# Performance work log

Hardware: AMD Instinct MI355X
Metric: run time of the kernel (lower is better)

The kernel has to match this reference:

```python
import jax, jax.numpy as jnp
import numpy as np

D_MODEL = 1024
N_HEADS = 16
HEAD_DIM = D_MODEL // N_HEADS
BATCH = 4
SEQ = 2048


def setup_inputs() -> dict:
    key = jax.random.key(0)
    k_x, k_wqkv, k_bqkv, k_wo, k_bo = jax.random.split(key, 5)
    x = jax.random.normal(k_x, (BATCH, SEQ, D_MODEL), dtype=jnp.float32)
    # causal mask: True = masked (upper triangle, excluding diagonal)
    mask = jnp.triu(jnp.ones((SEQ, SEQ), dtype=bool), k=1)
    lim = 1.0 / np.sqrt(D_MODEL)
    w_qkv = jax.random.uniform(k_wqkv, (D_MODEL, 3 * D_MODEL), jnp.float32, -lim, lim)
    b_qkv = jax.random.uniform(k_bqkv, (3 * D_MODEL,), jnp.float32, -lim, lim)
    w_out = jax.random.uniform(k_wo, (D_MODEL, D_MODEL), jnp.float32, -lim, lim)
    b_out = jax.random.uniform(k_bo, (D_MODEL,), jnp.float32, -lim, lim)
    return {"x": x, "mask": mask, "w_qkv": w_qkv, "b_qkv": b_qkv,
            "w_out": w_out, "b_out": b_out}


def reference(x, mask, w_qkv, b_qkv, w_out, b_out):
    b, s, _ = x.shape
    scale = HEAD_DIM ** -0.5
    qkv = x @ w_qkv + b_qkv                          # [b, s, 3*d]
    qkv = qkv.reshape(b, s, 3, N_HEADS, HEAD_DIM)
    qkv = jnp.transpose(qkv, (2, 0, 3, 1, 4))        # [3, b, h, s, hd]
    q, k, v = qkv[0], qkv[1], qkv[2]
    attn = jnp.einsum('bhqd,bhkd->bhqk', q, k) * scale
    attn = jnp.where(mask, -jnp.inf, attn)
    attn = jax.nn.softmax(attn, axis=-1)
    out = jnp.einsum('bhqk,bhkd->bhqd', attn, v)     # [b, h, s, hd]
    out = jnp.transpose(out, (0, 2, 1, 3)).reshape(b, s, D_MODEL)
    return out @ w_out + b_out
```

## Files before the change

kernel.cpp:

```cpp
#include <hip/hip_runtime.h>
#include <stdint.h>

typedef unsigned short u16;
typedef __attribute__((ext_vector_type(8))) short short8;
typedef __attribute__((ext_vector_type(4))) float f32x4;
typedef __attribute__((ext_vector_type(16))) float f32x16;

#define DEV static __device__ __forceinline__

#define QSCALE 0.18033688011112042f

DEV float fast_exp2(float x) { return __builtin_amdgcn_exp2f(x); }

DEV float bf2f(u16 u) { union { uint32_t i; float f; } x; x.i = ((uint32_t)u) << 16; return x.f; }
DEV u16 f2bf(float f) {
  union { float f; uint32_t i; } x; x.f = f;
  uint32_t r = x.i + 0x7FFFu + ((x.i >> 16) & 1u);
  return (u16)(r >> 16);
}
DEV uint32_t pk_bf16(float lo, float hi) {
  uint32_t r;
  asm("v_cvt_pk_bf16_f32 %0, %1, %2" : "=v"(r) : "v"(lo), "v"(hi));
  return r;
}

DEV void async_copy16(void* lds_dst, const void* gsrc) {
  typedef __attribute__((address_space(1))) void* gp_t;
  typedef __attribute__((address_space(3))) void* lp_t;
  __builtin_amdgcn_global_load_lds((gp_t)(uintptr_t)gsrc,
                                   (lp_t)(uint32_t)(uintptr_t)lds_dst, 16, 0, 0);
}

#define BUF_BYTES 49152

DEV void stage_slot(const u16* __restrict__ A, const u16* __restrict__ Bt,
                    int m0, int n0, int k0, uint8_t* buf, int tid) {
  uint8_t* As = buf;
  uint8_t* Bs = buf + 32768;
#pragma unroll
  for (int i = 0; i < 4; ++i) {
    int c = i * 512 + tid;
    int r = c >> 3;
    int ks = (c & 7) ^ (r & 7);
    async_copy16(As + c * 16, A + (size_t)(m0 + r) * 1024 + k0 + ks * 8);
  }
#pragma unroll
  for (int i = 0; i < 2; ++i) {
    int c = i * 512 + tid;
    int r = c >> 3;
    int ks = (c & 7) ^ (r & 7);
    async_copy16(Bs + c * 16, Bt + (size_t)(n0 + r) * 1024 + k0 + ks * 8);
  }
}

DEV void gemm256_core(const u16* __restrict__ A, const u16* __restrict__ Bt,
                      int m0, int n0, uint8_t* lds,
                      f32x4 (&acc)[4][4], int wave, int lane, int tid) {
  const int wm = (wave >> 1) * 64, wn = (wave & 1) * 64;
#pragma unroll
  for (int mf = 0; mf < 4; ++mf)
#pragma unroll
    for (int nf = 0; nf < 4; ++nf)
      acc[mf][nf] = (f32x4){0.f, 0.f, 0.f, 0.f};

  stage_slot(A, Bt, m0, n0, 0,  lds,             tid);
  stage_slot(A, Bt, m0, n0, 64, lds + BUF_BYTES, tid);
  asm volatile("s_waitcnt vmcnt(6)" ::: "memory");
  __builtin_amdgcn_s_barrier();

#pragma unroll 1
  for (int kt = 0; kt < 16; ++kt) {
    const uint8_t* Ab = lds + (kt & 1) * BUF_BYTES;
    const uint8_t* Bb = Ab + 32768;

    short8 a0[4], b0[4], a1[4], b1[4];
#pragma unroll
    for (int f = 0; f < 4; ++f) {
      int ra = wm + f * 16 + (lane & 15);
      int rb = wn + f * 16 + (lane & 15);
      a0[f] = *(const short8*)(Ab + ra * 128 + (((lane >> 4) ^ (ra & 7)) << 4));
      b0[f] = *(const short8*)(Bb + rb * 128 + (((lane >> 4) ^ (rb & 7)) << 4));
    }
#pragma unroll
    for (int f = 0; f < 4; ++f) {
      int ra = wm + f * 16 + (lane & 15);
      int rb = wn + f * 16 + (lane & 15);
      a1[f] = *(const short8*)(Ab + ra * 128 + (((4 + (lane >> 4)) ^ (ra & 7)) << 4));
      b1[f] = *(const short8*)(Bb + rb * 128 + (((4 + (lane >> 4)) ^ (rb & 7)) << 4));
    }

    asm volatile("s_waitcnt lgkmcnt(8)" ::: "memory");
    __builtin_amdgcn_sched_barrier(0);
    __builtin_amdgcn_s_setprio(1);
#pragma unroll
    for (int mf = 0; mf < 4; ++mf)
#pragma unroll
      for (int nf = 0; nf < 4; ++nf)
        acc[mf][nf] = __builtin_amdgcn_mfma_f32_16x16x32_bf16(a0[mf], b0[nf],
                                                              acc[mf][nf], 0, 0, 0);
    __builtin_amdgcn_s_setprio(0);

    asm volatile("s_waitcnt lgkmcnt(0)" ::: "memory");
    __builtin_amdgcn_sched_barrier(0);
    __builtin_amdgcn_s_barrier();

    if (kt + 2 < 16)
      stage_slot(A, Bt, m0, n0, (kt + 2) * 64, lds + (kt & 1) * BUF_BYTES, tid);

    __builtin_amdgcn_s_setprio(1);
#pragma unroll
    for (int mf = 0; mf < 4; ++mf)
#pragma unroll
      for (int nf = 0; nf < 4; ++nf)
        acc[mf][nf] = __builtin_amdgcn_mfma_f32_16x16x32_bf16(a1[mf], b1[nf],
                                                              acc[mf][nf], 0, 0, 0);
    __builtin_amdgcn_s_setprio(0);

    if (kt + 2 < 16) asm volatile("s_waitcnt vmcnt(6)" ::: "memory");
    else             asm volatile("s_waitcnt vmcnt(0)" ::: "memory");
    __builtin_amdgcn_s_barrier();
  }
}

__global__ __launch_bounds__(512, 2) void k_gemm_qkv(
    const u16* __restrict__ X, const u16* __restrict__ WT, const float* __restrict__ bias,
    u16* __restrict__ Q, u16* __restrict__ Kv, u16* __restrict__ Vt) {
  __shared__ __attribute__((aligned(16))) uint8_t lds[2 * BUF_BYTES];
  const int tid = threadIdx.x, lane = tid & 63, wave = tid >> 6;
  const int wm = (wave >> 1) * 64, wn = (wave & 1) * 64;
  const int m0 = blockIdx.x * 256, n0 = blockIdx.y * 128;
  f32x4 acc[4][4];
  gemm256_core(X, WT, m0, n0, lds, acc, wave, lane, tid);
#pragma unroll
  for (int nf = 0; nf < 4; ++nf) {
    int n = n0 + wn + nf * 16 + (lane & 15);
    float bv = bias[n];
    int which = n >> 10, h = (n >> 6) & 15, hd = n & 63;
    if (which == 2) {
#pragma unroll
      for (int mf = 0; mf < 4; ++mf) {
        int m = m0 + wm + mf * 16 + (lane >> 4) * 4;
        int b = m >> 11, s = m & 2047;
        u16 tmp[4];
#pragma unroll
        for (int rg = 0; rg < 4; ++rg) tmp[rg] = f2bf(acc[mf][nf][rg] + bv);
        *(uint64_t*)(Vt + ((size_t)(b * 16 + h) * 64 + hd) * 2048 + s) = *(const uint64_t*)tmp;
      }
    } else {
      u16* base = (which == 0) ? Q : Kv;
      const float mul = (which == 0) ? QSCALE : 1.0f;
#pragma unroll
      for (int mf = 0; mf < 4; ++mf)
#pragma unroll
        for (int rg = 0; rg < 4; ++rg) {
          int m = m0 + wm + mf * 16 + (lane >> 4) * 4 + rg;
          int b = m >> 11, s = m & 2047;
          base[((size_t)(b * 16 + h) * 2048 + s) * 64 + hd] = f2bf((acc[mf][nf][rg] + bv) * mul);
        }
    }
  }
}

__global__ __launch_bounds__(512, 2) void k_gemm_out(
    const u16* __restrict__ A, const u16* __restrict__ WT, const float* __restrict__ bias,
    float* __restrict__ Out) {
  __shared__ __attribute__((aligned(16))) uint8_t lds[2 * BUF_BYTES];
  const int tid = threadIdx.x, lane = tid & 63, wave = tid >> 6;
  const int wm = (wave >> 1) * 64, wn = (wave & 1) * 64;
  const int m0 = blockIdx.x * 256, n0 = blockIdx.y * 128;
  f32x4 acc[4][4];
  gemm256_core(A, WT, m0, n0, lds, acc, wave, lane, tid);
#pragma unroll
  for (int nf = 0; nf < 4; ++nf) {
    int n = n0 + wn + nf * 16 + (lane & 15);
    float bv = bias[n];
#pragma unroll
    for (int mf = 0; mf < 4; ++mf)
#pragma unroll
      for (int rg = 0; rg < 4; ++rg) {
        int m = m0 + wm + mf * 16 + (lane >> 4) * 4 + rg;
        Out[(size_t)m * 1024 + n] = acc[mf][nf][rg] + bv;
      }
  }
}

__global__ __launch_bounds__(256) void k_cvt_x(const float* __restrict__ src,
                                               u16* __restrict__ dst, int n8) {
  int i = blockIdx.x * 256 + threadIdx.x;
  if (i >= n8) return;
  float4 a = *(const float4*)(src + (size_t)i * 8);
  float4 b = *(const float4*)(src + (size_t)i * 8 + 4);
  u16 tmp[8] = {f2bf(a.x), f2bf(a.y), f2bf(a.z), f2bf(a.w),
                f2bf(b.x), f2bf(b.y), f2bf(b.z), f2bf(b.w)};
  *(short8*)(dst + (size_t)i * 8) = *(const short8*)tmp;
}

__global__ __launch_bounds__(256) void k_transpose_f32(
    const float* __restrict__ src, u16* __restrict__ dst, int R, int C) {
  __shared__ u16 tile[64][72];
  const int tr = blockIdx.x * 64, tc = blockIdx.y * 64;
  for (int c = threadIdx.x; c < 1024; c += 256) {
    int r = c >> 4, c4 = (c & 15) * 4;
    float4 v = *(const float4*)(src + (size_t)(tr + r) * C + tc + c4);
    tile[r][c4 + 0] = f2bf(v.x); tile[r][c4 + 1] = f2bf(v.y);
    tile[r][c4 + 2] = f2bf(v.z); tile[r][c4 + 3] = f2bf(v.w);
  }
  __syncthreads();
  for (int c = threadIdx.x; c < 512; c += 256) {
    int oc = c >> 3, r8 = (c & 7) * 8;
    u16 tmp[8];
#pragma unroll
    for (int i = 0; i < 8; ++i) tmp[i] = tile[r8 + i][oc];
    *(short8*)(dst + (size_t)(tc + oc) * R + tr + r8) = *(const short8*)tmp;
  }
}

DEV void stage_tile(const u16* __restrict__ Kg, const u16* __restrict__ Vg,
                    uint8_t* kb, uint8_t* vb, int t, int tid) {
#pragma unroll
  for (int i = 0; i < 2; ++i) {
    int c = i * 256 + tid;
    int r = c >> 3;
    int ks = (c & 7) ^ (r & 7);
    async_copy16(kb + c * 16, Kg + (size_t)(t * 64 + r) * 64 + ks * 8);
    async_copy16(vb + c * 16, Vg + (size_t)r * 2048 + t * 64 + ks * 8);
  }
}

__global__ __launch_bounds__(256, 2) void k_attn(
    const u16* __restrict__ Q, const u16* __restrict__ K,
    const u16* __restrict__ Vt, u16* __restrict__ O) {
  __shared__ __attribute__((aligned(16))) uint8_t kbuf[2][8192];
  __shared__ __attribute__((aligned(16))) uint8_t vbuf[2][8192];
  const int tid = threadIdx.x;
  const int lane = tid & 63;
  const int wave = tid >> 6;
  const int q32 = lane & 31, hv = lane >> 5;
  const float NEG_INF = -__builtin_inff();

  int L = blockIdx.x;
  int bh = (L & 7) * 8 + ((L >> 3) >> 3);
  int pair = (L >> 3) & 7;
  const int b = bh >> 4, h = bh & 15;
  const size_t hb = (size_t)bh * (2048 * 64);
  const u16* Qg = Q + hb;
  const u16* Kg = K + hb;
  const u16* Vg = Vt + hb;

#pragma unroll 1
  for (int which = 0; which < 2; ++which) {
    const int s = which ? (15 - pair) : pair;
    const int nt = 2 * (s + 1);
    const int qbase = s * 128 + wave * 32;
    const int qg = qbase + q32;
    const int my_nt = ((qbase + 31) >> 6) + 1;

    short8 qf[4];
#pragma unroll
    for (int dblk = 0; dblk < 4; ++dblk)
      qf[dblk] = *(const short8*)(Qg + (size_t)qg * 64 + dblk * 16 + hv * 8);

    f32x16 oacc[2] = {};
    float mrun = NEG_INF, lrun = 0.f;

    stage_tile(Kg, Vg, kbuf[0], vbuf[0], 0, tid);
    __syncthreads();

#pragma unroll 1
    for (int t = 0; t < nt; ++t) {
      const int cur = t & 1;
      if (t + 1 < nt) stage_tile(Kg, Vg, kbuf[cur ^ 1], vbuf[cur ^ 1], t + 1, tid);

      if (t < my_nt) {
        const uint8_t* kb = kbuf[cur];
        const uint8_t* vb = vbuf[cur];

        f32x16 sa0 = {}, sa1 = {};
        __builtin_amdgcn_s_setprio(1);
#pragma unroll
        for (int dblk = 0; dblk < 4; ++dblk) {
          short8 kf0 = *(const short8*)(kb + q32 * 128 + (((dblk * 2 + hv) ^ (q32 & 7)) << 4));
          short8 kf1 = *(const short8*)(kb + (32 + q32) * 128 + (((dblk * 2 + hv) ^ (q32 & 7)) << 4));
          sa0 = __builtin_amdgcn_mfma_f32_32x32x16_bf16(kf0, qf[dblk], sa0, 0, 0, 0);
          sa1 = __builtin_amdgcn_mfma_f32_32x32x16_bf16(kf1, qf[dblk], sa1, 0, 0, 0);
        }
        __builtin_amdgcn_s_setprio(0);

        float sv[32];
#pragma unroll
        for (int r = 0; r < 16; ++r) { sv[r] = sa0[r]; sv[16 + r] = sa1[r]; }
        if (t * 64 + 63 > qbase) {
#pragma unroll
          for (int r = 0; r < 16; ++r) {
            int kl = (r & 3) + 8 * (r >> 2) + 4 * hv;
            if (t * 64 + kl > qg)      sv[r]      = NEG_INF;
            if (t * 64 + 32 + kl > qg) sv[16 + r] = NEG_INF;
          }
        }

        float mloc = fmaxf(sv[0], sv[1]);
#pragma unroll
        for (int r = 2; r < 32; ++r) mloc = fmaxf(mloc, sv[r]);
        float mtile = fmaxf(mloc, __shfl_xor(mloc, 32, 64));
        if (!__all(mtile <= mrun + 8.f)) {
          float mnew = fmaxf(mrun, mtile);
          float corr = fast_exp2(mrun - mnew);
          mrun = mnew;
          lrun *= corr;
#pragma unroll
          for (int r = 0; r < 16; ++r) { oacc[0][r] *= corr; oacc[1][r] *= corr; }
        }
        float ls = 0.f;
#pragma unroll
        for (int r = 0; r < 32; ++r) { sv[r] = fast_exp2(sv[r] - mrun); ls += sv[r]; }
        ls += __shfl_xor(ls, 32, 64);
        lrun += ls;

        __builtin_amdgcn_s_setprio(1);
#pragma unroll
        for (int ksub = 0; ksub < 2; ++ksub) {
#pragma unroll
          for (int kb2 = 0; kb2 < 2; ++kb2) {
            const int rb = ksub * 16 + kb2 * 8;
            uint32_t pA = pk_bf16(sv[rb + 0], sv[rb + 1]);
            uint32_t pB = pk_bf16(sv[rb + 2], sv[rb + 3]);
            uint32_t pC = pk_bf16(sv[rb + 4], sv[rb + 5]);
            uint32_t pD = pk_bf16(sv[rb + 6], sv[rb + 7]);
            uint32_t X = hv ? pA : pC;
            uint32_t Y = hv ? pB : pD;
            uint32_t sX = (uint32_t)__shfl_xor((int)X, 32, 64);
            uint32_t sY = (uint32_t)__shfl_xor((int)Y, 32, 64);
            union { uint32_t u[4]; short8 s8; } pu;
            pu.u[0] = hv ? sX : pA;
            pu.u[1] = hv ? sY : pB;
            pu.u[2] = hv ? pC : sX;
            pu.u[3] = hv ? pD : sY;
            const int kblk = ksub * 2 + kb2;
            short8 vf0 = *(const short8*)(vb + q32 * 128 + (((kblk * 2 + hv) ^ (q32 & 7)) << 4));
            short8 vf1 = *(const short8*)(vb + (32 + q32) * 128 + (((kblk * 2 + hv) ^ (q32 & 7)) << 4));
            oacc[0] = __builtin_amdgcn_mfma_f32_32x32x16_bf16(vf0, pu.s8, oacc[0], 0, 0, 0);
            oacc[1] = __builtin_amdgcn_mfma_f32_32x32x16_bf16(vf1, pu.s8, oacc[1], 0, 0, 0);
          }
        }
        __builtin_amdgcn_s_setprio(0);
      }

      __syncthreads();
    }

    float rl = 1.0f / lrun;
    u16* orow = O + ((size_t)(b * 2048 + qg)) * 1024 + h * 64;
#pragma unroll
    for (int dt = 0; dt < 2; ++dt)
#pragma unroll
      for (int g = 0; g < 4; ++g) {
        int dbase = dt * 32 + 8 * g + 4 * hv;
        u16 tmp[4];
#pragma unroll
        for (int j2 = 0; j2 < 4; ++j2) tmp[j2] = f2bf(oacc[dt][4 * g + j2] * rl);
        *(uint64_t*)(orow + dbase) = *(const uint64_t*)tmp;
      }
  }
}

extern "C" void kernel_launch(void* const* d_in, const int* in_sizes, int n_in,
                              void* d_out, int out_size, void* d_ws, size_t ws_size,
                              hipStream_t stream) {
  const float* x     = (const float*)d_in[0];
  const float* w_qkv = (const float*)d_in[2];
  const float* b_qkv = (const float*)d_in[3];
  const float* w_out = (const float*)d_in[4];
  const float* b_out = (const float*)d_in[5];
  float* out = (float*)d_out;
  uint8_t* ws = (uint8_t*)d_ws;

  u16* wqkvT = (u16*)(ws);
  u16* woutT = (u16*)(ws +  6291456);
  u16* Xb    = (u16*)(ws +  8388608);
  u16* Qb    = (u16*)(ws + 25165824);
  u16* Kb    = (u16*)(ws + 41943040);
  u16* Vtb   = (u16*)(ws + 58720256);
  u16* AO    = Xb;

  k_cvt_x<<<dim3(4096), 256, 0, stream>>>(x, Xb, 1048576);
  k_transpose_f32<<<dim3(16, 48), 256, 0, stream>>>(w_qkv, wqkvT, 1024, 3072);
  k_transpose_f32<<<dim3(16, 16), 256, 0, stream>>>(w_out, woutT, 1024, 1024);
  k_gemm_qkv<<<dim3(32, 24), 512, 0, stream>>>(Xb, wqkvT, b_qkv, Qb, Kb, Vtb);
  k_attn<<<dim3(512), 256, 0, stream>>>(Qb, Kb, Vtb, AO);
  k_gemm_out<<<dim3(32, 8), 512, 0, stream>>>(AO, woutT, b_out, out);
}
```

Before: 160.6 us.

## Use simpler 128x128 single-buffered GEMM core for QKV projection

Replaces the QKV projection's 256x128 double-buffered, prefetching GEMM core with a new 128x128-tile core. The new core uses 256 threads and a single LDS buffer with a barrier on each side of every K-step, and the grid doubles along M. It drops the software pipelining and the wave priority hints, so global loads no longer overlap MFMA work, in exchange for more blocks and less LDS per block.

```diff
diff --git a/kernel.cpp b/kernel.cpp
--- a/kernel.cpp
+++ b/kernel.cpp
@@ -29,6 +29,49 @@
   typedef __attribute__((address_space(3))) void* lp_t;
   __builtin_amdgcn_global_load_lds((gp_t)(uintptr_t)gsrc,
                                    (lp_t)(uint32_t)(uintptr_t)lds_dst, 16, 0, 0);
+}
+
+DEV void gemm_bt_core(const u16* __restrict__ A, const u16* __restrict__ Bt, int K,
+                      int m0, int n0, uint8_t* As, uint8_t* Bs,
+                      f32x4 (&acc)[4][4], int wave, int lane, int wm, int wn) {
+#pragma unroll
+  for (int mt = 0; mt < 4; ++mt)
+#pragma unroll
+    for (int nt = 0; nt < 4; ++nt)
+      acc[mt][nt] = (f32x4){0.f, 0.f, 0.f, 0.f};
+
+  for (int k0 = 0; k0 < K; k0 += 64) {
+    __syncthreads();
+#pragma unroll
+    for (int i = 0; i < 4; ++i) {
+      int cb = wave * 256 + i * 64;
+      int c  = cb + lane;
+      int r  = c >> 3;
+      int ks = (c & 7) ^ (r & 7);
+      async_copy16(As + cb * 16 + lane * 16, A  + (size_t)(m0 + r) * K + k0 + ks * 8);
+      async_copy16(Bs + cb * 16 + lane * 16, Bt + (size_t)(n0 + r) * K + k0 + ks * 8);
+    }
+    __syncthreads();
+
+    short8 af[2][4], bf_[2][4];
+#pragma unroll
+    for (int kk = 0; kk < 2; ++kk)
+#pragma unroll
+      for (int t = 0; t < 4; ++t) {
+        int ra = wm + t * 16 + (lane & 15);
+        af[kk][t]  = *(const short8*)(As + ra * 128 + (((kk * 4 + (lane >> 4)) ^ (ra & 7)) << 4));
+        int rb = wn + t * 16 + (lane & 15);
+        bf_[kk][t] = *(const short8*)(Bs + rb * 128 + (((kk * 4 + (lane >> 4)) ^ (rb & 7)) << 4));
+      }
+#pragma unroll
+    for (int kk = 0; kk < 2; ++kk)
+#pragma unroll
+      for (int mt = 0; mt < 4; ++mt)
+#pragma unroll
+        for (int nt = 0; nt < 4; ++nt)
+          acc[mt][nt] = __builtin_amdgcn_mfma_f32_16x16x32_bf16(af[kk][mt], bf_[kk][nt],
+                                                                acc[mt][nt], 0, 0, 0);
+  }
 }
 
 #define BUF_BYTES 49152
@@ -122,40 +165,41 @@
   }
 }
 
-__global__ __launch_bounds__(512, 2) void k_gemm_qkv(
+__global__ __launch_bounds__(256, 2) void k_gemm_qkv(
     const u16* __restrict__ X, const u16* __restrict__ WT, const float* __restrict__ bias,
     u16* __restrict__ Q, u16* __restrict__ Kv, u16* __restrict__ Vt) {
-  __shared__ __attribute__((aligned(16))) uint8_t lds[2 * BUF_BYTES];
-  const int tid = threadIdx.x, lane = tid & 63, wave = tid >> 6;
+  __shared__ __attribute__((aligned(16))) uint8_t As[16384];
+  __shared__ __attribute__((aligned(16))) uint8_t Bs[16384];
+  const int lane = threadIdx.x & 63, wave = threadIdx.x >> 6;
   const int wm = (wave >> 1) * 64, wn = (wave & 1) * 64;
-  const int m0 = blockIdx.x * 256, n0 = blockIdx.y * 128;
+  const int m0 = blockIdx.x * 128, n0 = blockIdx.y * 128;
   f32x4 acc[4][4];
-  gemm256_core(X, WT, m0, n0, lds, acc, wave, lane, tid);
-#pragma unroll
-  for (int nf = 0; nf < 4; ++nf) {
-    int n = n0 + wn + nf * 16 + (lane & 15);
+  gemm_bt_core(X, WT, 1024, m0, n0, As, Bs, acc, wave, lane, wm, wn);
+#pragma unroll
+  for (int nt = 0; nt < 4; ++nt) {
+    int n = n0 + wn + nt * 16 + (lane & 15);
     float bv = bias[n];
     int which = n >> 10, h = (n >> 6) & 15, hd = n & 63;
     if (which == 2) {
 #pragma unroll
-      for (int mf = 0; mf < 4; ++mf) {
-        int m = m0 + wm + mf * 16 + (lane >> 4) * 4;
+      for (int mt = 0; mt < 4; ++mt) {
+        int m = m0 + wm + mt * 16 + (lane >> 4) * 4;
         int b = m >> 11, s = m & 2047;
         u16 tmp[4];
 #pragma unroll
-        for (int rg = 0; rg < 4; ++rg) tmp[rg] = f2bf(acc[mf][nf][rg] + bv);
+        for (int rg = 0; rg < 4; ++rg) tmp[rg] = f2bf(acc[mt][nt][rg] + bv);
         *(uint64_t*)(Vt + ((size_t)(b * 16 + h) * 64 + hd) * 2048 + s) = *(const uint64_t*)tmp;
       }
     } else {
       u16* base = (which == 0) ? Q : Kv;
       const float mul = (which == 0) ? QSCALE : 1.0f;
 #pragma unroll
-      for (int mf = 0; mf < 4; ++mf)
+      for (int mt = 0; mt < 4; ++mt)
 #pragma unroll
         for (int rg = 0; rg < 4; ++rg) {
-          int m = m0 + wm + mf * 16 + (lane >> 4) * 4 + rg;
+          int m = m0 + wm + mt * 16 + (lane >> 4) * 4 + rg;
           int b = m >> 11, s = m & 2047;
-          base[((size_t)(b * 16 + h) * 2048 + s) * 64 + hd] = f2bf((acc[mf][nf][rg] + bv) * mul);
+          base[((size_t)(b * 16 + h) * 2048 + s) * 64 + hd] = f2bf((acc[mt][nt][rg] + bv) * mul);
         }
     }
   }
@@ -385,7 +429,7 @@
   k_cvt_x<<<dim3(4096), 256, 0, stream>>>(x, Xb, 1048576);
   k_transpose_f32<<<dim3(16, 48), 256, 0, stream>>>(w_qkv, wqkvT, 1024, 3072);
   k_transpose_f32<<<dim3(16, 16), 256, 0, stream>>>(w_out, woutT, 1024, 1024);
-  k_gemm_qkv<<<dim3(32, 24), 512, 0, stream>>>(Xb, wqkvT, b_qkv, Qb, Kb, Vtb);
+  k_gemm_qkv<<<dim3(64, 24), 256, 0, stream>>>(Xb, wqkvT, b_qkv, Qb, Kb, Vtb);
   k_attn<<<dim3(512), 256, 0, stream>>>(Qb, Kb, Vtb, AO);
   k_gemm_out<<<dim3(32, 8), 512, 0, stream>>>(AO, woutT, b_out, out);
 }
```

Result: faster. 155.0 us (-3.5%).
